# Kernel tuning notes

Hardware: AMD Instinct MI355X
Metric: run time of the kernel (lower is better)

## Reference

```python
import jax, jax.numpy as jnp
import numpy as np

H = 8  # num_heads
LN_EPS = 1e-5


def setup_inputs() -> dict:
    key = jax.random.key(0)
    ks = jax.random.split(key, 12)
    B, N, D = 1, 4096, 256
    E = 65536
    x = jax.random.normal(ks[0], (B, N, D), dtype=jnp.float32)
    # random edges + self-loops so every row of the mask has >=1 True (avoids NaN softmax)
    src = jax.random.randint(ks[1], (E,), 0, N)
    dst = jax.random.randint(ks[2], (E,), 0, N)
    loop = jnp.arange(N)
    edge_index = jnp.stack([jnp.concatenate([src, loop]),
                            jnp.concatenate([dst, loop])]).astype(jnp.int64)  # [2, 69632]
    s = 1.0 / np.sqrt(D)
    Wq = jax.random.normal(ks[3], (D, D), dtype=jnp.float32) * s
    Wk = jax.random.normal(ks[4], (D, D), dtype=jnp.float32) * s
    Wv = jax.random.normal(ks[5], (D, D), dtype=jnp.float32) * s
    Wo = jax.random.normal(ks[6], (D, D), dtype=jnp.float32) * s
    bq = jax.random.normal(ks[7], (D,), dtype=jnp.float32) * 0.01
    bk = jax.random.normal(ks[8], (D,), dtype=jnp.float32) * 0.01
    bv = jax.random.normal(ks[9], (D,), dtype=jnp.float32) * 0.01
    bo = jax.random.normal(ks[10], (D,), dtype=jnp.float32) * 0.01
    gamma = jnp.ones((D,), dtype=jnp.float32)
    beta = jnp.zeros((D,), dtype=jnp.float32)
    return {"x": x, "edge_index": edge_index, "Wq": Wq, "bq": bq, "Wk": Wk, "bk": bk,
            "Wv": Wv, "bv": bv, "Wo": Wo, "bo": bo, "gamma": gamma, "beta": beta}


def reference(x, edge_index, Wq, bq, Wk, bk, Wv, bv, Wo, bo, gamma, beta):
    B, N, D = x.shape
    hd = D // H
    # QKV projections -> [B, H, N, hd]
    def proj(W, b):
        return (x @ W + b).reshape(B, N, H, hd).transpose(0, 2, 1, 3)
    Q, K, V = proj(Wq, bq), proj(Wk, bk), proj(Wv, bv)
    scores = jnp.einsum('bhnd,bhmd->bhnm', Q, K) / jnp.sqrt(jnp.float32(hd))
    # dense boolean adjacency mask scattered from edge list
    mask = jnp.zeros((N, N), dtype=bool).at[edge_index[0], edge_index[1]].set(True)
    scores = jnp.where(mask[None, None], scores, -jnp.inf)
    attn = jax.nn.softmax(scores, axis=-1)  # dropout is identity in eval mode
    attended = jnp.einsum('bhnm,bhmd->bhnd', attn, V)
    attended = attended.transpose(0, 2, 1, 3).reshape(B, N, D)
    out = attended @ Wo + bo
    y = x + out
    mu = jnp.mean(y, axis=-1, keepdims=True)
    var = jnp.mean((y - mu) ** 2, axis=-1, keepdims=True)
    return (y - mu) / jnp.sqrt(var + LN_EPS) * gamma + beta
```

## Files before the change

kernel.cpp:

```cpp
#include <hip/hip_runtime.h>

#define N_NODES 4096
#define DMODEL  256
#define NHEAD   8
#define HDIM    32
#define LN_EPS  1e-5f
#define MAXDEG  64

typedef __attribute__((ext_vector_type(8))) short short8;
typedef __attribute__((ext_vector_type(4))) float f32x4;

__device__ __forceinline__ unsigned short f2bf(float f) {
  unsigned int x = __float_as_uint(f);
  x += 0x7fffu + ((x >> 16) & 1u);
  return (unsigned short)(x >> 16);
}
__device__ __forceinline__ float bf2f(unsigned short u) {
  return __uint_as_float(((unsigned int)u) << 16);
}

__global__ __launch_bounds__(256) void prep_kernel(
    const float* __restrict__ w0, const float* __restrict__ w1,
    const float* __restrict__ w2, const float* __restrict__ w3,
    unsigned short* __restrict__ wt,
    const int* __restrict__ e0, const int* __restrict__ e1, int ne, int eb,
    unsigned int* __restrict__ bits, int* __restrict__ cnt) {
  __shared__ float t[32][33];
  int bid = blockIdx.x, tid = threadIdx.x;
  if (bid < 256) {
    int kbi = bid & 7, nbi = (bid >> 3) & 7, m = bid >> 6;
    const float* w = (m == 0) ? w0 : (m == 1) ? w1 : (m == 2) ? w2 : w3;
    int tx = tid & 31, ty = tid >> 5;
    int kb = kbi * 32, nb = nbi * 32;
#pragma unroll
    for (int r = 0; r < 32; r += 8)
      t[ty + r][tx] = w[(kb + ty + r) * 256 + nb + tx];
    __syncthreads();
    unsigned short* o = wt + m * 65536;
#pragma unroll
    for (int r = 0; r < 32; r += 8)
      o[(nb + ty + r) * 256 + kb + tx] = f2bf(t[tx][ty + r]);
  } else if (bid < 256 + eb) {
    int i = (bid - 256) * 256 + tid;
    if (i < ne) {
      unsigned int bitpos = ((unsigned int)e0[i] << 12) | (unsigned int)e1[i];
      bits[bitpos >> 5] = 0u;
    }
  } else {
    cnt[(bid - 256 - eb) * 256 + tid] = 0;
  }
}

__global__ __launch_bounds__(512) void qkv_scatter(
    const float* __restrict__ x, const unsigned short* __restrict__ wt,
    const float* __restrict__ bq, const float* __restrict__ bk,
    const float* __restrict__ bv,
    const int* __restrict__ e0, const int* __restrict__ e1, int ne,
    unsigned int* __restrict__ bits, int* __restrict__ cnt,
    int* __restrict__ colidx,
    unsigned short* __restrict__ Qb, unsigned short* __restrict__ Kb,
    unsigned short* __restrict__ Vb) {
  int bid = blockIdx.x, tid = threadIdx.x;
  if (bid >= 256) {
    int i = (bid - 256) * 512 + tid;
    if (i < ne) {
      int s = e0[i], d = e1[i];
      unsigned int bitpos = ((unsigned int)s << 12) | (unsigned int)d;
      unsigned int word = bitpos >> 5, msk = 1u << (bitpos & 31);
      unsigned int old = atomicOr(&bits[word], msk);
      if (!(old & msk)) {
        int pos = atomicAdd(&cnt[s], 1);
        if (pos < MAXDEG) colidx[s * MAXDEG + pos] = d;
      }
    }
    return;
  }
  int lane = tid & 63, w = tid >> 6;
  int Mbase = bid * 16;
  int arow = lane & 15, kgrp = lane >> 4;
  short8 a[8];
  const float* ab = x + (Mbase + arow) * 256 + kgrp * 8;
#pragma unroll
  for (int kk = 0; kk < 8; ++kk) {
    float4 v0 = *reinterpret_cast<const float4*>(ab + kk * 32);
    float4 v1 = *reinterpret_cast<const float4*>(ab + kk * 32 + 4);
    short8 tv;
    tv[0] = (short)f2bf(v0.x); tv[1] = (short)f2bf(v0.y);
    tv[2] = (short)f2bf(v0.z); tv[3] = (short)f2bf(v0.w);
    tv[4] = (short)f2bf(v1.x); tv[5] = (short)f2bf(v1.y);
    tv[6] = (short)f2bf(v1.z); tv[7] = (short)f2bf(v1.w);
    a[kk] = tv;
  }
#pragma unroll
  for (int mat = 0; mat < 3; ++mat) {
    const unsigned short* wm = wt + mat * 65536;
    const float* bias_p = (mat == 0) ? bq : (mat == 1) ? bk : bv;
    unsigned short* o = (mat == 0) ? Qb : (mat == 1) ? Kb : Vb;
#pragma unroll
    for (int nf = 0; nf < 2; ++nf) {
      int col = w * 32 + nf * 16 + arow;
      const unsigned short* bb = wm + col * 256 + kgrp * 8;
      f32x4 acc = {0.f, 0.f, 0.f, 0.f};
#pragma unroll
      for (int kk = 0; kk < 8; ++kk) {
        short8 b = *reinterpret_cast<const short8*>(bb + kk * 32);
        acc = __builtin_amdgcn_mfma_f32_16x16x32_bf16(a[kk], b, acc, 0, 0, 0);
      }
      float bias = bias_p[col];
#pragma unroll
      for (int r = 0; r < 4; ++r) {
        int row = Mbase + kgrp * 4 + r;
        o[row * 256 + col] = f2bf(acc[r] + bias);
      }
    }
  }
}

__global__ __launch_bounds__(1024, 1) void attn_out_ln(
    const unsigned short* __restrict__ Qb, const unsigned short* __restrict__ Kb,
    const unsigned short* __restrict__ Vb, const int* __restrict__ cnt,
    const int* __restrict__ colidx, const unsigned short* __restrict__ wot,
    const float* __restrict__ bo, const float* __restrict__ x,
    const float* __restrict__ gamma, const float* __restrict__ beta,
    float* __restrict__ out) {
  __shared__ unsigned short att_lds[16][264];
  __shared__ float ylds[16][260];
  __shared__ float ps[16][65], pq[16][65];
  __shared__ float mu_s[16], ri_s[16];

  int tid = threadIdx.x;
  int Mbase = blockIdx.x * 16;
  const float scale = 0.17677669529663687f;

  {
    int g = tid >> 3;
    int gl = tid & 7;
    int ni = g >> 3, h = g & 7;
    int n = Mbase + ni;

    float qf[32];
    {
      const short8* q8 = reinterpret_cast<const short8*>(Qb + n * 256 + h * 32);
#pragma unroll
      for (int b = 0; b < 4; ++b) {
        short8 qv = q8[b];
#pragma unroll
        for (int j = 0; j < 8; ++j) qf[b * 8 + j] = bf2f((unsigned short)qv[j]) * scale;
      }
    }

    int deg = cnt[n]; deg = (deg > MAXDEG) ? MAXDEG : deg;
    const int* nbrs = colidx + n * MAXDEG;

    float s[8]; int c[8];
#pragma unroll
    for (int i = 0; i < 8; ++i) { s[i] = -3.0e38f; c[i] = 0; }
#pragma unroll
    for (int i = 0; i < 8; ++i) {
      if (8 * i >= deg) break;
      int idx = 8 * i + gl;
      if (idx < deg) {
        c[i] = nbrs[idx];
        const short8* k8 = reinterpret_cast<const short8*>(Kb + c[i] * 256 + h * 32);
        float d = 0.f;
#pragma unroll
        for (int b = 0; b < 4; ++b) {
          short8 kv = k8[b];
#pragma unroll
          for (int j = 0; j < 8; ++j)
            d += qf[b * 8 + j] * bf2f((unsigned short)kv[j]);
        }
        s[i] = d;
      }
    }

    float gm = s[0];
#pragma unroll
    for (int i = 1; i < 8; ++i) gm = fmaxf(gm, s[i]);
    gm = fmaxf(gm, __shfl_xor(gm, 1, 8));
    gm = fmaxf(gm, __shfl_xor(gm, 2, 8));
    gm = fmaxf(gm, __shfl_xor(gm, 4, 8));

    float l = 0.f;
#pragma unroll
    for (int i = 0; i < 8; ++i) {
      if (8 * i >= deg) break;
      s[i] = __expf(s[i] - gm);
      l += s[i];
    }
    l += __shfl_xor(l, 1, 8);
    l += __shfl_xor(l, 2, 8);
    l += __shfl_xor(l, 4, 8);

    float a0 = 0.f, a1 = 0.f, a2 = 0.f, a3 = 0.f;
#pragma unroll
    for (int i = 0; i < 8; ++i) {
      if (8 * i >= deg) break;
#pragma unroll
      for (int lj = 0; lj < 8; ++lj) {
        if (8 * i + lj >= deg) break;
        float pj = __shfl(s[i], lj, 8);
        int cj = __shfl(c[i], lj, 8);
        ushort4 vv = *reinterpret_cast<const ushort4*>(Vb + cj * 256 + h * 32 + gl * 4);
        a0 += pj * bf2f(vv.x);
        a1 += pj * bf2f(vv.y);
        a2 += pj * bf2f(vv.z);
        a3 += pj * bf2f(vv.w);
      }
    }
    float rl = 1.f / l;
    ushort4 pkt;
    pkt.x = f2bf(a0 * rl); pkt.y = f2bf(a1 * rl);
    pkt.z = f2bf(a2 * rl); pkt.w = f2bf(a3 * rl);
    *reinterpret_cast<ushort4*>(&att_lds[ni][h * 32 + gl * 4]) = pkt;
  }
  __syncthreads();

  {
    int lane = tid & 63, w = tid >> 6;
    int arow = lane & 15, kgrp = lane >> 4;

    short8 a[8];
#pragma unroll
    for (int kk = 0; kk < 8; ++kk)
      a[kk] = *reinterpret_cast<const short8*>(&att_lds[arow][kgrp * 8 + kk * 32]);

    int col = w * 16 + arow;
    const unsigned short* bb = wot + col * 256 + kgrp * 8;
    f32x4 acc = {0.f, 0.f, 0.f, 0.f};
#pragma unroll
    for (int kk = 0; kk < 8; ++kk) {
      short8 b = *reinterpret_cast<const short8*>(bb + kk * 32);
      acc = __builtin_amdgcn_mfma_f32_16x16x32_bf16(a[kk], b, acc, 0, 0, 0);
    }
    float bof = bo[col];
#pragma unroll
    for (int r = 0; r < 4; ++r) {
      int row = kgrp * 4 + r;
      float xv = x[(Mbase + row) * 256 + col];
      ylds[row][col] = acc[r] + bof + xv;
    }
  }
  __syncthreads();

  int r = tid >> 6, seg = tid & 63;
  float sm = 0.f, sq = 0.f;
#pragma unroll
  for (int j = 0; j < 4; ++j) {
    float v = ylds[r][seg * 4 + j];
    sm += v;
    sq += v * v;
  }
  ps[r][seg] = sm;
  pq[r][seg] = sq;
  __syncthreads();
  if (tid < 16) {
    float S = 0.f, Q2 = 0.f;
#pragma unroll
    for (int cc = 0; cc < 64; ++cc) { S += ps[tid][cc]; Q2 += pq[tid][cc]; }
    float mu = S * (1.f / 256.f);
    float var = Q2 * (1.f / 256.f) - mu * mu;
    mu_s[tid] = mu;
    ri_s[tid] = rsqrtf(var + LN_EPS);
  }
  __syncthreads();
  float mu = mu_s[r], ri = ri_s[r];
  float* orow = out + (Mbase + r) * 256;
#pragma unroll
  for (int j = 0; j < 4; ++j) {
    int cc = seg * 4 + j;
    float v = (ylds[r][cc] - mu) * ri * gamma[cc] + beta[cc];
    orow[cc] = v;
  }
}

extern "C" void kernel_launch(void* const* d_in, const int* in_sizes, int n_in,
                              void* d_out, int out_size, void* d_ws, size_t ws_size,
                              hipStream_t stream) {
  const float* x     = (const float*)d_in[0];
  const int*   edges = (const int*)d_in[1];
  const float* Wq    = (const float*)d_in[2];
  const float* bq    = (const float*)d_in[3];
  const float* Wk    = (const float*)d_in[4];
  const float* bk    = (const float*)d_in[5];
  const float* Wv    = (const float*)d_in[6];
  const float* bv    = (const float*)d_in[7];
  const float* Wo    = (const float*)d_in[8];
  const float* bo    = (const float*)d_in[9];
  const float* gamma = (const float*)d_in[10];
  const float* beta  = (const float*)d_in[11];
  float* out = (float*)d_out;
  int NE = in_sizes[1] / 2;
  int EB256 = (NE + 255) / 256;
  int EB512 = (NE + 511) / 512;

  char* p = (char*)d_ws;
  auto carve = [&](size_t sz) { char* r = p; p += ((sz + 255) / 256) * 256; return r; };
  unsigned short* Wt   = (unsigned short*)carve(4 * 65536 * sizeof(unsigned short));
  unsigned short* Qb   = (unsigned short*)carve((size_t)N_NODES * DMODEL * sizeof(unsigned short));
  unsigned short* Kb   = (unsigned short*)carve((size_t)N_NODES * DMODEL * sizeof(unsigned short));
  unsigned short* Vb   = (unsigned short*)carve((size_t)N_NODES * DMODEL * sizeof(unsigned short));
  unsigned int*   bits = (unsigned int*)carve((size_t)N_NODES * N_NODES / 8);
  int*            cnt  = (int*)carve(N_NODES * sizeof(int));
  int*            colidx = (int*)carve((size_t)N_NODES * MAXDEG * sizeof(int));

  prep_kernel<<<256 + EB256 + 16, 256, 0, stream>>>(Wq, Wk, Wv, Wo, Wt,
                                                    edges, edges + NE, NE, EB256, bits, cnt);
  qkv_scatter<<<256 + EB512, 512, 0, stream>>>(x, Wt, bq, bk, bv,
                                               edges, edges + NE, NE, bits, cnt, colidx,
                                               Qb, Kb, Vb);
  attn_out_ln<<<256, 1024, 0, stream>>>(Qb, Kb, Vb, cnt, colidx, Wt + 3 * 65536,
                                        bo, x, gamma, beta, out);
}
```

Before: 57.85 us.

## Drop prep kernel: read fp32 weights directly and build per-block adjacency in LDS

```diff
diff --git a/kernel.cpp b/kernel.cpp
--- a/kernel.cpp
+++ b/kernel.cpp
@@ -19,91 +19,61 @@
   return __uint_as_float(((unsigned int)u) << 16);
 }
 
-__global__ __launch_bounds__(256) void prep_kernel(
-    const float* __restrict__ w0, const float* __restrict__ w1,
-    const float* __restrict__ w2, const float* __restrict__ w3,
-    unsigned short* __restrict__ wt,
-    const int* __restrict__ e0, const int* __restrict__ e1, int ne, int eb,
-    unsigned int* __restrict__ bits, int* __restrict__ cnt) {
-  __shared__ float t[32][33];
-  int bid = blockIdx.x, tid = threadIdx.x;
-  if (bid < 256) {
-    int kbi = bid & 7, nbi = (bid >> 3) & 7, m = bid >> 6;
-    const float* w = (m == 0) ? w0 : (m == 1) ? w1 : (m == 2) ? w2 : w3;
-    int tx = tid & 31, ty = tid >> 5;
-    int kb = kbi * 32, nb = nbi * 32;
-#pragma unroll
-    for (int r = 0; r < 32; r += 8)
-      t[ty + r][tx] = w[(kb + ty + r) * 256 + nb + tx];
-    __syncthreads();
-    unsigned short* o = wt + m * 65536;
-#pragma unroll
-    for (int r = 0; r < 32; r += 8)
-      o[(nb + ty + r) * 256 + kb + tx] = f2bf(t[tx][ty + r]);
-  } else if (bid < 256 + eb) {
-    int i = (bid - 256) * 256 + tid;
-    if (i < ne) {
-      unsigned int bitpos = ((unsigned int)e0[i] << 12) | (unsigned int)e1[i];
-      bits[bitpos >> 5] = 0u;
-    }
-  } else {
-    cnt[(bid - 256 - eb) * 256 + tid] = 0;
-  }
-}
-
-__global__ __launch_bounds__(512) void qkv_scatter(
-    const float* __restrict__ x, const unsigned short* __restrict__ wt,
-    const float* __restrict__ bq, const float* __restrict__ bk,
-    const float* __restrict__ bv,
+__device__ __forceinline__ short8 wfrag(const float* __restrict__ W,
+                                        int kbase, int col) {
+  const float* wp = W + (size_t)kbase * 256 + col;
+  short8 b;
+#pragma unroll
+  for (int j = 0; j < 8; ++j) b[j] = (short)f2bf(wp[j * 256]);
+  return b;
+}
+
+__global__ __launch_bounds__(1024, 1) void qkv_csr(
+    const float* __restrict__ x,
+    const float* __restrict__ Wq, const float* __restrict__ bq,
+    const float* __restrict__ Wk, const float* __restrict__ bk,
+    const float* __restrict__ Wv, const float* __restrict__ bv,
     const int* __restrict__ e0, const int* __restrict__ e1, int ne,
-    unsigned int* __restrict__ bits, int* __restrict__ cnt,
-    int* __restrict__ colidx,
+    int* __restrict__ cnt, int* __restrict__ colidx,
     unsigned short* __restrict__ Qb, unsigned short* __restrict__ Kb,
     unsigned short* __restrict__ Vb) {
-  int bid = blockIdx.x, tid = threadIdx.x;
-  if (bid >= 256) {
-    int i = (bid - 256) * 512 + tid;
-    if (i < ne) {
-      int s = e0[i], d = e1[i];
-      unsigned int bitpos = ((unsigned int)s << 12) | (unsigned int)d;
-      unsigned int word = bitpos >> 5, msk = 1u << (bitpos & 31);
-      unsigned int old = atomicOr(&bits[word], msk);
-      if (!(old & msk)) {
-        int pos = atomicAdd(&cnt[s], 1);
-        if (pos < MAXDEG) colidx[s * MAXDEG + pos] = d;
-      }
-    }
-    return;
-  }
-  int lane = tid & 63, w = tid >> 6;
-  int Mbase = bid * 16;
-  int arow = lane & 15, kgrp = lane >> 4;
-  short8 a[8];
-  const float* ab = x + (Mbase + arow) * 256 + kgrp * 8;
-#pragma unroll
-  for (int kk = 0; kk < 8; ++kk) {
-    float4 v0 = *reinterpret_cast<const float4*>(ab + kk * 32);
-    float4 v1 = *reinterpret_cast<const float4*>(ab + kk * 32 + 4);
-    short8 tv;
-    tv[0] = (short)f2bf(v0.x); tv[1] = (short)f2bf(v0.y);
-    tv[2] = (short)f2bf(v0.z); tv[3] = (short)f2bf(v0.w);
-    tv[4] = (short)f2bf(v1.x); tv[5] = (short)f2bf(v1.y);
-    tv[6] = (short)f2bf(v1.z); tv[7] = (short)f2bf(v1.w);
-    a[kk] = tv;
-  }
-#pragma unroll
-  for (int mat = 0; mat < 3; ++mat) {
-    const unsigned short* wm = wt + mat * 65536;
-    const float* bias_p = (mat == 0) ? bq : (mat == 1) ? bk : bv;
-    unsigned short* o = (mat == 0) ? Qb : (mat == 1) ? Kb : Vb;
-#pragma unroll
-    for (int nf = 0; nf < 2; ++nf) {
-      int col = w * 32 + nf * 16 + arow;
-      const unsigned short* bb = wm + col * 256 + kgrp * 8;
+  __shared__ unsigned int bm[16 * 128];
+  __shared__ int lcnt[16];
+
+  const int tid = threadIdx.x;
+  const int bid = blockIdx.x;
+  const int Mbase = bid * 16;
+
+  for (int i = tid; i < 2048; i += 1024) bm[i] = 0u;
+  if (tid < 16) lcnt[tid] = 0;
+  __syncthreads();
+
+  {
+    int lane = tid & 63, w = tid >> 6;
+    int arow = lane & 15, kgrp = lane >> 4;
+    short8 a[8];
+    const float* ab = x + (Mbase + arow) * 256 + kgrp * 8;
+#pragma unroll
+    for (int kk = 0; kk < 8; ++kk) {
+      float4 v0 = *reinterpret_cast<const float4*>(ab + kk * 32);
+      float4 v1 = *reinterpret_cast<const float4*>(ab + kk * 32 + 4);
+      short8 tv;
+      tv[0] = (short)f2bf(v0.x); tv[1] = (short)f2bf(v0.y);
+      tv[2] = (short)f2bf(v0.z); tv[3] = (short)f2bf(v0.w);
+      tv[4] = (short)f2bf(v1.x); tv[5] = (short)f2bf(v1.y);
+      tv[6] = (short)f2bf(v1.z); tv[7] = (short)f2bf(v1.w);
+      a[kk] = tv;
+    }
+    int col = w * 16 + arow;
+#pragma unroll
+    for (int mat = 0; mat < 3; ++mat) {
+      const float* W = (mat == 0) ? Wq : (mat == 1) ? Wk : Wv;
+      const float* bias_p = (mat == 0) ? bq : (mat == 1) ? bk : bv;
+      unsigned short* o = (mat == 0) ? Qb : (mat == 1) ? Kb : Vb;
       f32x4 acc = {0.f, 0.f, 0.f, 0.f};
 #pragma unroll
       for (int kk = 0; kk < 8; ++kk) {
-        short8 b = *reinterpret_cast<const short8*>(bb + kk * 32);
+        short8 b = wfrag(W, kk * 32 + kgrp * 8, col);
         acc = __builtin_amdgcn_mfma_f32_16x16x32_bf16(a[kk], b, acc, 0, 0, 0);
       }
       float bias = bias_p[col];
@@ -114,12 +84,28 @@
       }
     }
   }
+
+  for (int i = tid; i < ne; i += 1024) {
+    int s = e0[i];
+    if ((s >> 4) == bid) {
+      int d = e1[i];
+      int li = s & 15;
+      unsigned int msk = 1u << (d & 31);
+      unsigned int old = atomicOr(&bm[li * 128 + (d >> 5)], msk);
+      if (!(old & msk)) {
+        int pos = atomicAdd(&lcnt[li], 1);
+        if (pos < MAXDEG) colidx[s * MAXDEG + pos] = d;
+      }
+    }
+  }
+  __syncthreads();
+  if (tid < 16) cnt[Mbase + tid] = lcnt[tid];
 }
 
 __global__ __launch_bounds__(1024, 1) void attn_out_ln(
     const unsigned short* __restrict__ Qb, const unsigned short* __restrict__ Kb,
     const unsigned short* __restrict__ Vb, const int* __restrict__ cnt,
-    const int* __restrict__ colidx, const unsigned short* __restrict__ wot,
+    const int* __restrict__ colidx, const float* __restrict__ Wo,
     const float* __restrict__ bo, const float* __restrict__ x,
     const float* __restrict__ gamma, const float* __restrict__ beta,
     float* __restrict__ out) {
@@ -145,7 +131,8 @@
       for (int b = 0; b < 4; ++b) {
         short8 qv = q8[b];
 #pragma unroll
-        for (int j = 0; j < 8; ++j) qf[b * 8 + j] = bf2f((unsigned short)qv[j]) * scale;
+        for (int j = 0; j < 8; ++j)
+          qf[b * 8 + j] = bf2f((unsigned short)qv[j]) * scale;
       }
     }
 
@@ -226,11 +213,10 @@
       a[kk] = *reinterpret_cast<const short8*>(&att_lds[arow][kgrp * 8 + kk * 32]);
 
     int col = w * 16 + arow;
-    const unsigned short* bb = wot + col * 256 + kgrp * 8;
     f32x4 acc = {0.f, 0.f, 0.f, 0.f};
 #pragma unroll
     for (int kk = 0; kk < 8; ++kk) {
-      short8 b = *reinterpret_cast<const short8*>(bb + kk * 32);
+      short8 b = wfrag(Wo, kk * 32 + kgrp * 8, col);
       acc = __builtin_amdgcn_mfma_f32_16x16x32_bf16(a[kk], b, acc, 0, 0, 0);
     }
     float bof = bo[col];
@@ -291,24 +277,18 @@
   const float* beta  = (const float*)d_in[11];
   float* out = (float*)d_out;
   int NE = in_sizes[1] / 2;
-  int EB256 = (NE + 255) / 256;
-  int EB512 = (NE + 511) / 512;
 
   char* p = (char*)d_ws;
   auto carve = [&](size_t sz) { char* r = p; p += ((sz + 255) / 256) * 256; return r; };
-  unsigned short* Wt   = (unsigned short*)carve(4 * 65536 * sizeof(unsigned short));
   unsigned short* Qb   = (unsigned short*)carve((size_t)N_NODES * DMODEL * sizeof(unsigned short));
   unsigned short* Kb   = (unsigned short*)carve((size_t)N_NODES * DMODEL * sizeof(unsigned short));
   unsigned short* Vb   = (unsigned short*)carve((size_t)N_NODES * DMODEL * sizeof(unsigned short));
-  unsigned int*   bits = (unsigned int*)carve((size_t)N_NODES * N_NODES / 8);
   int*            cnt  = (int*)carve(N_NODES * sizeof(int));
   int*            colidx = (int*)carve((size_t)N_NODES * MAXDEG * sizeof(int));
 
-  prep_kernel<<<256 + EB256 + 16, 256, 0, stream>>>(Wq, Wk, Wv, Wo, Wt,
-                                                    edges, edges + NE, NE, EB256, bits, cnt);
-  qkv_scatter<<<256 + EB512, 512, 0, stream>>>(x, Wt, bq, bk, bv,
-                                               edges, edges + NE, NE, bits, cnt, colidx,
-                                               Qb, Kb, Vb);
-  attn_out_ln<<<256, 1024, 0, stream>>>(Qb, Kb, Vb, cnt, colidx, Wt + 3 * 65536,
+  qkv_csr<<<256, 1024, 0, stream>>>(x, Wq, bq, Wk, bk, Wv, bv,
+                                    edges, edges + NE, NE, cnt, colidx,
+                                    Qb, Kb, Vb);
+  attn_out_ln<<<256, 1024, 0, stream>>>(Qb, Kb, Vb, cnt, colidx, Wo,
                                         bo, x, gamma, beta, out);
 }
```

Result: slower. 70.46 us (+21.8%).
